# Kernel optimization log

Hardware: AMD Instinct MI355X
Metric: run time of the kernel (lower is better)

## Reference

```python
import jax, jax.numpy as jnp
import numpy as np

EPS = 1e-8
LN_EPS = 1e-5

def _ln(x, g, b):
    m = x.mean(-1, keepdims=True)
    v = ((x - m) ** 2).mean(-1, keepdims=True)
    return (x - m) * jax.lax.rsqrt(v + LN_EPS) * g + b

def _rbf(d, n_rbf):
    # standard protein RBF embedding: gaussians on [0, 20] Angstrom
    mu = jnp.linspace(0.0, 20.0, n_rbf)
    sigma = 20.0 / n_rbf
    return jnp.exp(-(((d[..., None] - mu) / sigma) ** 2))

def setup_inputs() -> dict:
    N, K, CS, CZ, G, RBF = 1024, 16, 256, 128, 16, 64
    key = jax.random.key(0)
    ks = jax.random.split(key, 24)
    s = 0.02
    inp = {
        'node_features': jax.random.normal(ks[0], (N, CS), jnp.float32),
        'trans': jax.random.normal(ks[1], (N, 3), jnp.float32) * 10.0,
        'src_edge_features': jax.random.normal(ks[2], (N, K, CZ), jnp.float32),
        'dst_edge_features': jax.random.normal(ks[3], (N, K, CZ), jnp.float32),
        # params
        'ln_src_g': jnp.ones((CZ,)), 'ln_src_b': jnp.zeros((CZ,)),
        'ln_dst_g': jnp.ones((CZ,)), 'ln_dst_b': jnp.zeros((CZ,)),
        'W_nl': jax.random.normal(ks[4], (G, CS)) * s, 'b_nl': jnp.zeros((G,)),
        'W_nr': jax.random.normal(ks[5], (G, CS)) * s, 'b_nr': jnp.zeros((G,)),
        'W_ep': jax.random.normal(ks[6], (CZ, CZ)) * s, 'b_ep': jnp.zeros((CZ,)),
        'W_eg': jax.random.normal(ks[7], (CZ, CZ)) * s, 'b_eg': jnp.zeros((CZ,)),
        'W_dg': jax.random.normal(ks[8], (CZ, G, G)) * s, 'b_dg': jnp.zeros((CZ,)),
        'W_dp': jax.random.normal(ks[9], (CZ, RBF)) * s, 'b_dp': jnp.zeros((CZ,)),
        'ln_out_g': jnp.ones((CZ,)), 'ln_out_b': jnp.zeros((CZ,)),
        'W_lo': jax.random.normal(ks[10], (CZ, CZ)) * s, 'b_lo': jnp.zeros((CZ,)),
        'W_og': jax.random.normal(ks[11], (CZ, CZ)) * s, 'b_og': jnp.zeros((CZ,)),
        # int / mask args (KNN form)
        'src_edge_index': jax.random.randint(ks[12], (2, N, K), 0, N, jnp.int32),
        'dst_edge_index': jax.random.randint(ks[13], (2, N, K), 0, N, jnp.int32),
        'src_mask': jnp.ones((N, K), bool),
        'dst_mask': jnp.ones((N, K), bool),
    }
    return inp

def reference(node_features, trans, src_edge_features, dst_edge_features,
              ln_src_g, ln_src_b, ln_dst_g, ln_dst_b,
              W_nl, b_nl, W_nr, b_nr, W_ep, b_ep, W_eg, b_eg,
              W_dg, b_dg, W_dp, b_dp, ln_out_g, ln_out_b,
              W_lo, b_lo, W_og, b_og,
              src_edge_index, dst_edge_index, src_mask, dst_mask):
    N, K, CZ = src_edge_features.shape
    src_ln = _ln(src_edge_features, ln_src_g, ln_src_b)   # [N,K,CZ]
    dst_ln = _ln(dst_edge_features, ln_dst_g, ln_dst_b)
    node_left = node_features @ W_nl.T + b_nl              # [N,G]
    node_right = node_features @ W_nr.T + b_nr
    e1 = node_left[src_edge_index[0]]                      # [N,K,G]
    e2 = node_right[dst_edge_index[0]]                     # [N,K,G]
    # triangle gate: fuse outer product [N,K,K,G,G] with dist_gate Linear
    t = jnp.einsum('nia,zab->nizb', e1, W_dg)
    gate3 = jnp.einsum('nizb,njb->nijz', t, e2) + b_dg     # [N,K,K,CZ]
    t1 = trans[src_edge_index[0]]                          # [N,K,3]
    t2 = trans[dst_edge_index[0]]
    d = jnp.linalg.norm(t1[:, :, None, :] - t2[:, None, :, :] + EPS, axis=-1)  # [N,K,K]
    distf = _rbf(d, W_dp.shape[1]) @ W_dp.T + b_dp         # [N,K,K,CZ]
    mask3 = (src_mask[:, :, None] & dst_mask[:, None, :])[..., None]
    edge3 = jax.nn.sigmoid(gate3) * distf * mask3          # [N,K,K,CZ]
    edge2 = jax.nn.sigmoid(src_ln @ W_eg.T + b_eg) * (src_ln @ W_ep.T + b_ep)  # [N,K,CZ]
    # batched per-channel combine: sum over dst slot j
    upd = jnp.einsum('nijz,njz->niz', edge3, edge2)        # [N,K,CZ]
    upd = _ln(upd, ln_out_g, ln_out_b) @ W_lo.T + b_lo
    upd = upd * jax.nn.sigmoid(dst_ln @ W_og.T + b_og)
    upd = upd * dst_mask[..., None]                        # knn -> sparse (masked flatten)
    return upd.reshape(N * K, CZ)
```

## Files before the change

### kernel.cpp

```cpp
#include <hip/hip_runtime.h>
#include <hip/hip_bf16.h>
#include <stdint.h>

#define N_    1024
#define K_    16
#define CZ_   128
#define G_    16
#define RBF_  64
#define CS_   256

typedef const float* fp;
typedef _Float16 f16x8 __attribute__((ext_vector_type(8)));
typedef _Float16 h2    __attribute__((ext_vector_type(2)));
typedef float f32x4    __attribute__((ext_vector_type(4)));

#define MFMA16(A,B,C) __builtin_amdgcn_mfma_f32_16x16x32_f16(A,B,C,0,0,0)

#define OFF_EGH 0
#define OFF_EPH 16384
#define OFF_OGH 32768
#define OFF_LOH 49152
#define OFF_DPH 65536
#define OFF_DGA 73728

__device__ __forceinline__ float sigm(float x){
  return __builtin_amdgcn_rcpf(1.0f + __expf(-x));
}
__device__ __forceinline__ unsigned short f2h(float v){
  union{_Float16 h; unsigned short u;} c; c.h = (_Float16)v; return c.u;
}
__device__ __forceinline__ float h2f(unsigned short u){
  union{unsigned short u; _Float16 h;} c; c.u = u; return (float)c.h;
}
__device__ __forceinline__ unsigned int pk2(float a, float b){
  union{h2 h; unsigned int u;} c; c.h[0] = (_Float16)a; c.h[1] = (_Float16)b; return c.u;
}
__device__ __forceinline__ f16x8 ldh8(const unsigned short* p){
  union{uint4 u; f16x8 h;} c; c.u = *(const uint4*)p; return c.h;
}
__device__ __forceinline__ f16x8 ldh8u(const unsigned short* p){
  union{uint2 u[2]; f16x8 h;} c;
  c.u[0] = *(const uint2*)p;
  c.u[1] = *(const uint2*)(p+4);
  return c.h;
}
__device__ __forceinline__ f16x8 cvt8(float4 a, float4 b){
  f16x8 r;
  r[0]=(_Float16)a.x; r[1]=(_Float16)a.y; r[2]=(_Float16)a.z; r[3]=(_Float16)a.w;
  r[4]=(_Float16)b.x; r[5]=(_Float16)b.y; r[6]=(_Float16)b.z; r[7]=(_Float16)b.w;
  return r;
}

__global__ __launch_bounds__(256) void repack(
    fp W_eg, fp W_ep, fp W_og, fp W_lo, fp W_dp, fp W_dg,
    unsigned short* __restrict__ ws)
{
  int t = blockIdx.x*256 + threadIdx.x;
  int stride = gridDim.x*256;
  for (int i = t; i < 16384; i += stride) {
    ws[OFF_EGH+i] = f2h(W_eg[i]);
    ws[OFF_EPH+i] = f2h(W_ep[i]);
    ws[OFF_OGH+i] = f2h(W_og[i]);
    ws[OFF_LOH+i] = f2h(W_lo[i]);
  }
  for (int i = t; i < 8192; i += stride)
    ws[OFF_DPH+i] = f2h(W_dp[i]);
  for (int i = t; i < 32768; i += stride) {
    int z = i >> 8, rem = i & 255;
    int l = rem >> 3, c = rem & 7;
    int a = ((l >> 4) << 3) | c;
    int b = l & 15;
    ws[OFF_DGA+i] = f2h(W_dg[z*256 + a*16 + b]);
  }
}

__global__ __launch_bounds__(512, 4) void tri_fused6(
    fp nf, fp trans, fp srcef, fp dstef,
    fp ln_src_g, fp ln_src_b, fp ln_dst_g, fp ln_dst_b,
    fp W_nl, fp b_nl, fp W_nr, fp b_nr,
    fp b_eg, fp b_ep, fp b_og,
    fp b_dg, fp b_dp, fp ln_out_g, fp ln_out_b, fp b_lo,
    const int* __restrict__ sidx, const int* __restrict__ didx,
    const unsigned short* __restrict__ ws,
    float* __restrict__ out)
{
  __shared__ __align__(16) unsigned char smem[72192];
  float*          updf   = (float*)smem;
  unsigned short* edge2h = (unsigned short*)(smem + 8448);
  unsigned short* sogh   = (unsigned short*)(smem + 13056);
  unsigned short* e1h    = (unsigned short*)(smem + 17152);
  unsigned short* e2h    = (unsigned short*)(smem + 17664);
  float (*t1f)[4]        = (float(*)[4])(smem + 18304);
  float (*t2f)[4]        = (float(*)[4])(smem + 18560);
  unsigned short* poolH  = (unsigned short*)(smem + 18816);
  unsigned short* srcH   = poolH;
  unsigned short* dstH   = poolH + 2176;
  unsigned short* t_lds  = poolH;
  unsigned short* rbfH   = poolH + 16448;
  unsigned short* updH   = poolH;

  const int n   = blockIdx.x;
  const int tid = threadIdx.x;
  const int wv  = tid >> 6;
  const int lnn = tid & 63;
  const int lm  = lnn & 15;
  const int lq  = lnn >> 4;
  const int zz0 = wv*16 + lm;

  const int pf_which = wv & 1;
  const int pf_h     = wv >> 1;
  int pf_idx = (pf_which ? didx : sidx)[n*K_ + lm];
  const float* pf_arow = nf + pf_idx*CS_ + pf_h*64 + lq*8;
  const float* pf_wrow = (pf_which ? W_nr : W_nl) + lm*CS_ + pf_h*64 + lq*8;
  float4 pa0 = *(const float4*)(pf_arow);
  float4 pa1 = *(const float4*)(pf_arow + 4);
  float4 pa2 = *(const float4*)(pf_arow + 32);
  float4 pa3 = *(const float4*)(pf_arow + 36);
  float4 pw0 = *(const float4*)(pf_wrow);
  float4 pw1 = *(const float4*)(pf_wrow + 4);
  float4 pw2 = *(const float4*)(pf_wrow + 32);
  float4 pw3 = *(const float4*)(pf_wrow + 36);
  f16x8 wegv0 = ldh8(ws + OFF_EGH + zz0*128 + lq*8);
  f16x8 weph0 = ldh8(ws + OFF_EPH + zz0*128 + lq*8);
  f16x8 wogv0 = ldh8(ws + OFF_OGH + zz0*128 + lq*8);

  if (tid < 32) {
    int k = tid & 15;
    int id2 = (tid < 16) ? sidx[n*K_ + k] : didx[n*K_ + k];
    float* tf = (tid < 16) ? &t1f[k][0] : &t2f[k][0];
    tf[0] = trans[id2*3+0]; tf[1] = trans[id2*3+1]; tf[2] = trans[id2*3+2];
  }
  {
    int row = tid >> 4;
    int c0  = (tid & 15) * 8;
    int r16 = row & 15;
    bool isSrc = row < 16;
    const float* base = (isSrc ? srcef : dstef) + (n*K_ + r16)*CZ_ + c0;
    float4 xa = *(const float4*)base;
    float4 xb = *(const float4*)(base+4);
    float x[8] = {xa.x,xa.y,xa.z,xa.w,xb.x,xb.y,xb.z,xb.w};
    float s = x[0]+x[1]+x[2]+x[3]+x[4]+x[5]+x[6]+x[7];
    s += __shfl_xor(s,1); s += __shfl_xor(s,2);
    s += __shfl_xor(s,4); s += __shfl_xor(s,8);
    float m = s * 0.0078125f;
    float q = 0.f;
    #pragma unroll
    for (int i = 0; i < 8; ++i) { float d = x[i]-m; q += d*d; }
    q += __shfl_xor(q,1); q += __shfl_xor(q,2);
    q += __shfl_xor(q,4); q += __shfl_xor(q,8);
    float rv = rsqrtf(q * 0.0078125f + 1e-5f);
    fp gp = isSrc ? ln_src_g : ln_dst_g;
    fp bp = isSrc ? ln_src_b : ln_dst_b;
    float y[8];
    #pragma unroll
    for (int i = 0; i < 8; ++i) y[i] = (x[i]-m)*rv*gp[c0+i] + bp[c0+i];
    uint4 uh;
    uh.x = pk2(y[0],y[1]); uh.y = pk2(y[2],y[3]); uh.z = pk2(y[4],y[5]); uh.w = pk2(y[6],y[7]);
    *(uint4*)&((isSrc ? srcH : dstH)[r16*136 + c0]) = uh;
  }
  __syncthreads();

  {
    f32x4 acc = {0.f,0.f,0.f,0.f};
    acc = MFMA16(cvt8(pa0,pa1), cvt8(pw0,pw1), acc);
    acc = MFMA16(cvt8(pa2,pa3), cvt8(pw2,pw3), acc);
    float* pst = (float*)updf;
    #pragma unroll
    for (int r = 0; r < 4; ++r)
      pst[wv*256 + r*64 + lnn] = acc[r];
  }

  {
    const int z = zz0;
    f32x4 aeg = {0.f,0.f,0.f,0.f}, aep = {0.f,0.f,0.f,0.f}, aog = {0.f,0.f,0.f,0.f};
    {
      f16x8 sh = ldh8(srcH + lm*136 + lq*8);
      f16x8 dh = ldh8(dstH + lm*136 + lq*8);
      aeg = MFMA16(sh, wegv0, aeg);
      aep = MFMA16(sh, weph0, aep);
      aog = MFMA16(dh, wogv0, aog);
    }
    #pragma unroll
    for (int kb = 32; kb < 128; kb += 32) {
      f16x8 sh = ldh8(srcH + lm*136 + kb + lq*8);
      f16x8 dh = ldh8(dstH + lm*136 + kb + lq*8);
      f16x8 wegv = ldh8(ws + OFF_EGH + z*128 + kb + lq*8);
      f16x8 weph = ldh8(ws + OFF_EPH + z*128 + kb + lq*8);
      f16x8 wogv = ldh8(ws + OFF_OGH + z*128 + kb + lq*8);
      aeg = MFMA16(sh, wegv, aeg);
      aep = MFMA16(sh, weph, aep);
      aog = MFMA16(dh, wogv, aog);
    }
    float beg = b_eg[z], bep = b_ep[z], bog = b_og[z];
    #pragma unroll
    for (int r = 0; r < 4; ++r) {
      int j = lq*4 + r;
      edge2h[z*18 + j] = f2h(sigm(aeg[r]+beg) * (aep[r]+bep));
      sogh[j*128 + z]  = f2h(sigm(aog[r]+bog));
    }
  }
  __syncthreads();

  if (wv < 2) {
    const float* pst = (const float*)updf;
    float bias = (wv ? b_nr : b_nl)[lm];
    #pragma unroll
    for (int r = 0; r < 4; ++r) {
      float v = pst[(wv  )*256 + r*64 + lnn]
              + pst[(wv+2)*256 + r*64 + lnn]
              + pst[(wv+4)*256 + r*64 + lnn]
              + pst[(wv+6)*256 + r*64 + lnn];
      v += bias;
      if (wv) e2h[(lq*4+r)*20 + lm] = f2h(v);
      else    e1h[(lq*4+r)*16 + lm] = f2h(v);
    }
  }
  __syncthreads();

  {
    const int z = zz0;
    f16x8 Bdp0 = ldh8(ws + OFF_DPH + z*64 + lq*8);
    f16x8 Bdp1 = ldh8(ws + OFF_DPH + z*64 + 32 + lq*8);
    const float bdg = b_dg[z], bdp = b_dp[z];
    float e2v4[4];
    #pragma unroll
    for (int r = 0; r < 4; ++r) e2v4[r] = h2f(edge2h[z*18 + lq*4 + r]);

    f16x8 zf = {(_Float16)0,(_Float16)0,(_Float16)0,(_Float16)0,
                (_Float16)0,(_Float16)0,(_Float16)0,(_Float16)0};
    f16x8 e1B = zf;
    f16x8 e2A = zf;
    if (lq < 2) {
      e1B = ldh8 (e1h + lm*16 + lq*8);
      e2A = ldh8u(e2h + lm*20 + lq*8);
    }
    const float inv_sigma = 3.2f;
    const float mustep = 20.0f/63.0f;

    for (int h = 0; h < 2; ++h) {
      __syncthreads();
      for (int zz = 0; zz < 16; ++zz) {
        int za = wv*16 + zz;
        f16x8 Ad = zf;
        if (lnn < 32) Ad = ldh8(ws + OFF_DGA + za*256 + lnn*8);
        f32x4 d4 = MFMA16(Ad, e1B, ((f32x4){0.f,0.f,0.f,0.f}));
        if ((lm >> 3) == h) {
          int ii = lm & 7;
          uint2 u;
          u.x = pk2(d4[0], d4[1]);
          u.y = pk2(d4[2], d4[3]);
          *(uint2*)&t_lds[ii*2056 + za*16 + lq*4] = u;
        }
      }
      {
        const int kh = wv & 1;
        #pragma unroll
        for (int p = 0; p < 2; ++p) {
          int slot = (wv >> 1) + p*4;
          int i = h*8 + slot;
          float dx = t1f[i][0]-t2f[lm][0]+1e-8f;
          float dy = t1f[i][1]-t2f[lm][1]+1e-8f;
          float dz = t1f[i][2]-t2f[lm][2]+1e-8f;
          float d = sqrtf(dx*dx+dy*dy+dz*dz);
          union { f16x8 hh; uint2 u2[2]; } cv;
          #pragma unroll
          for (int c = 0; c < 8; ++c) {
            int k = kh*32 + lq*8 + c;
            float tt = (d - (float)k*mustep) * inv_sigma;
            cv.hh[c] = (_Float16)__expf(-tt*tt);
          }
          unsigned short* dp = &rbfH[(slot*64+lnn)*20 + kh*8];
          *(uint2*)dp     = cv.u2[0];
          *(uint2*)(dp+4) = cv.u2[1];
        }
      }
      __syncthreads();

      for (int ii = 0; ii < 8; ++ii) {
        int i = h*8 + ii;
        f16x8 tB = zf;
        if (lq < 2) tB = ldh8(t_lds + ii*2056 + z*16 + lq*8);
        f32x4 accg = MFMA16(e2A, tB, ((f32x4){0.f,0.f,0.f,0.f}));
        const unsigned short* rp = &rbfH[(ii*64+lnn)*20];
        f16x8 r0 = ldh8u(rp);
        f16x8 r1 = ldh8u(rp + 8);
        f32x4 accp = {0.f,0.f,0.f,0.f};
        accp = MFMA16(r0, Bdp0, accp);
        accp = MFMA16(r1, Bdp1, accp);
        float s = 0.f;
        #pragma unroll
        for (int r = 0; r < 4; ++r)
          s += sigm(accg[r]+bdg) * (accp[r]+bdp) * e2v4[r];
        s += __shfl_xor(s,16); s += __shfl_xor(s,32);
        if (lq == 0) updf[i*132 + z] = s;
      }
    }
  }
  __syncthreads();

  {
    int row = tid >> 5;
    int c0  = (tid & 31) * 4;
    float4 x = *(const float4*)&updf[row*132 + c0];
    float s = x.x+x.y+x.z+x.w;
    s += __shfl_xor(s,1,32); s += __shfl_xor(s,2,32); s += __shfl_xor(s,4,32);
    s += __shfl_xor(s,8,32); s += __shfl_xor(s,16,32);
    float m = s * 0.0078125f;
    float q = (x.x-m)*(x.x-m)+(x.y-m)*(x.y-m)+(x.z-m)*(x.z-m)+(x.w-m)*(x.w-m);
    q += __shfl_xor(q,1,32); q += __shfl_xor(q,2,32); q += __shfl_xor(q,4,32);
    q += __shfl_xor(q,8,32); q += __shfl_xor(q,16,32);
    float rv = rsqrtf(q*0.0078125f + 1e-5f);
    float y0 = (x.x-m)*rv*ln_out_g[c0+0] + ln_out_b[c0+0];
    float y1 = (x.y-m)*rv*ln_out_g[c0+1] + ln_out_b[c0+1];
    float y2 = (x.z-m)*rv*ln_out_g[c0+2] + ln_out_b[c0+2];
    float y3 = (x.w-m)*rv*ln_out_g[c0+3] + ln_out_b[c0+3];
    uint2 uh;
    uh.x = pk2(y0,y1); uh.y = pk2(y2,y3);
    *(uint2*)&updH[row*136 + c0] = uh;
  }
  __syncthreads();

  {
    const int z = zz0;
    f32x4 acc = {0.f,0.f,0.f,0.f};
    #pragma unroll
    for (int kb = 0; kb < 128; kb += 32) {
      f16x8 ah = ldh8(updH + lm*136 + kb + lq*8);
      f16x8 bh = ldh8(ws + OFF_LOH + z*128 + kb + lq*8);
      acc = MFMA16(ah, bh, acc);
    }
    float blo = b_lo[z];
    #pragma unroll
    for (int r = 0; r < 4; ++r) {
      int islot = lq*4 + r;
      out[(n*K_ + islot)*CZ_ + z] = (acc[r] + blo) * h2f(sogh[islot*128 + z]);
    }
  }
}

extern "C" void kernel_launch(void* const* d_in, const int* in_sizes, int n_in,
                              void* d_out, int out_size, void* d_ws, size_t ws_size,
                              hipStream_t stream)
{
  fp nodef    = (fp)d_in[0];
  fp trans    = (fp)d_in[1];
  fp srcef    = (fp)d_in[2];
  fp dstef    = (fp)d_in[3];
  fp ln_src_g = (fp)d_in[4];  fp ln_src_b = (fp)d_in[5];
  fp ln_dst_g = (fp)d_in[6];  fp ln_dst_b = (fp)d_in[7];
  fp W_nl = (fp)d_in[8];   fp b_nl = (fp)d_in[9];
  fp W_nr = (fp)d_in[10];  fp b_nr = (fp)d_in[11];
  fp W_ep = (fp)d_in[12];  fp b_ep = (fp)d_in[13];
  fp W_eg = (fp)d_in[14];  fp b_eg = (fp)d_in[15];
  fp W_dg = (fp)d_in[16];  fp b_dg = (fp)d_in[17];
  fp W_dp = (fp)d_in[18];  fp b_dp = (fp)d_in[19];
  fp ln_out_g = (fp)d_in[20]; fp ln_out_b = (fp)d_in[21];
  fp W_lo = (fp)d_in[22];  fp b_lo = (fp)d_in[23];
  fp W_og = (fp)d_in[24];  fp b_og = (fp)d_in[25];
  const int* sidx = (const int*)d_in[26];
  const int* didx = (const int*)d_in[27];

  unsigned short* ws16 = (unsigned short*)d_ws;
  float* outp = (float*)d_out;

  hipLaunchKernelGGL(repack, dim3(64), dim3(256), 0, stream,
                     W_eg, W_ep, W_og, W_lo, W_dp, W_dg, ws16);
  hipLaunchKernelGGL(tri_fused6, dim3(N_), dim3(512), 0, stream,
                     nodef, trans, srcef, dstef,
                     ln_src_g, ln_src_b, ln_dst_g, ln_dst_b,
                     W_nl, b_nl, W_nr, b_nr,
                     b_eg, b_ep, b_og,
                     b_dg, b_dp, ln_out_g, ln_out_b, b_lo,
                     sidx, didx, ws16, outp);
}
```

Measured before the change: 182.4 us.

## Double-buffer triangle-gate and RBF staging across quarters to overlap producer and consumer

Splits the 16 source slots into four quarters with ping-pong LDS buffers for the gate intermediate and the RBF tiles. The next quarter's gate MFMAs and RBF exp computation are interleaved with the current quarter's consume MFMAs, so each quarter needs one barrier instead of two per half. The aim is to hide LDS write, barrier and transcendental latency behind MFMA work. In exchange, the stage-A gate MFMAs are now recomputed per quarter rather than per half, roughly doubling that work, and the LDS pool is packed to the full allocation.

```diff
diff --git a/kernel.cpp b/kernel.cpp
--- a/kernel.cpp
+++ b/kernel.cpp
@@ -95,8 +95,10 @@
   unsigned short* poolH  = (unsigned short*)(smem + 18816);
   unsigned short* srcH   = poolH;
   unsigned short* dstH   = poolH + 2176;
-  unsigned short* t_lds  = poolH;
-  unsigned short* rbfH   = poolH + 16448;
+  unsigned short* t0p    = poolH;
+  unsigned short* rbf0p  = poolH + 8224;
+  unsigned short* t1p    = poolH + 13344;
+  unsigned short* rbf1p  = poolH + 21568;
   unsigned short* updH   = poolH;
 
   const int n   = blockIdx.x;
@@ -237,66 +239,82 @@
     const float inv_sigma = 3.2f;
     const float mustep = 20.0f/63.0f;
 
-    for (int h = 0; h < 2; ++h) {
-      __syncthreads();
-      for (int zz = 0; zz < 16; ++zz) {
+    auto stageA4 = [&](int qq, unsigned short* tp, int k4) {
+      #pragma unroll
+      for (int zz = k4*4; zz < k4*4+4; ++zz) {
         int za = wv*16 + zz;
         f16x8 Ad = zf;
         if (lnn < 32) Ad = ldh8(ws + OFF_DGA + za*256 + lnn*8);
         f32x4 d4 = MFMA16(Ad, e1B, ((f32x4){0.f,0.f,0.f,0.f}));
-        if ((lm >> 3) == h) {
-          int ii = lm & 7;
+        if ((lm >> 2) == qq) {
+          int ii = lm & 3;
           uint2 u;
           u.x = pk2(d4[0], d4[1]);
           u.y = pk2(d4[2], d4[3]);
-          *(uint2*)&t_lds[ii*2056 + za*16 + lq*4] = u;
+          *(uint2*)&tp[ii*2056 + za*16 + lq*4] = u;
         }
       }
-      {
-        const int kh = wv & 1;
+    };
+    auto produceR = [&](int qq, unsigned short* rp) {
+      const int kh = wv & 1;
+      int slot = wv >> 1;
+      int i = qq*4 + slot;
+      float dx = t1f[i][0]-t2f[lm][0]+1e-8f;
+      float dy = t1f[i][1]-t2f[lm][1]+1e-8f;
+      float dz = t1f[i][2]-t2f[lm][2]+1e-8f;
+      float d = sqrtf(dx*dx+dy*dy+dz*dz);
+      union { f16x8 hh; uint2 u2[2]; } cv;
+      #pragma unroll
+      for (int c = 0; c < 8; ++c) {
+        int k = kh*32 + lq*8 + c;
+        float tt = (d - (float)k*mustep) * inv_sigma;
+        cv.hh[c] = (_Float16)__expf(-tt*tt);
+      }
+      unsigned short* dp = &rp[(slot*64+lnn)*20 + kh*8];
+      *(uint2*)dp     = cv.u2[0];
+      *(uint2*)(dp+4) = cv.u2[1];
+    };
+    auto consumeB = [&](int q, int ii, unsigned short* tc, unsigned short* rc) {
+      int i = q*4 + ii;
+      f16x8 tB = zf;
+      if (lq < 2) tB = ldh8(tc + ii*2056 + z*16 + lq*8);
+      f32x4 accg = MFMA16(e2A, tB, ((f32x4){0.f,0.f,0.f,0.f}));
+      const unsigned short* rr = &rc[(ii*64+lnn)*20];
+      f16x8 r0 = ldh8u(rr);
+      f16x8 r1 = ldh8u(rr + 8);
+      f32x4 accp = {0.f,0.f,0.f,0.f};
+      accp = MFMA16(r0, Bdp0, accp);
+      accp = MFMA16(r1, Bdp1, accp);
+      float s = 0.f;
+      #pragma unroll
+      for (int r = 0; r < 4; ++r)
+        s += sigm(accg[r]+bdg) * (accp[r]+bdp) * e2v4[r];
+      s += __shfl_xor(s,16); s += __shfl_xor(s,32);
+      if (lq == 0) updf[i*132 + z] = s;
+    };
+
+    stageA4(0, t0p, 0); stageA4(0, t0p, 1); stageA4(0, t0p, 2); stageA4(0, t0p, 3);
+    produceR(0, rbf0p);
+    __syncthreads();
+    for (int q = 0; q < 4; ++q) {
+      unsigned short* tc = (q & 1) ? t1p  : t0p;
+      unsigned short* rc = (q & 1) ? rbf1p: rbf0p;
+      unsigned short* tp = (q & 1) ? t0p  : t1p;
+      unsigned short* rp = (q & 1) ? rbf0p: rbf1p;
+      if (q < 3) {
         #pragma unroll
-        for (int p = 0; p < 2; ++p) {
-          int slot = (wv >> 1) + p*4;
-          int i = h*8 + slot;
-          float dx = t1f[i][0]-t2f[lm][0]+1e-8f;
-          float dy = t1f[i][1]-t2f[lm][1]+1e-8f;
-          float dz = t1f[i][2]-t2f[lm][2]+1e-8f;
-          float d = sqrtf(dx*dx+dy*dy+dz*dz);
-          union { f16x8 hh; uint2 u2[2]; } cv;
-          #pragma unroll
-          for (int c = 0; c < 8; ++c) {
-            int k = kh*32 + lq*8 + c;
-            float tt = (d - (float)k*mustep) * inv_sigma;
-            cv.hh[c] = (_Float16)__expf(-tt*tt);
-          }
-          unsigned short* dp = &rbfH[(slot*64+lnn)*20 + kh*8];
-          *(uint2*)dp     = cv.u2[0];
-          *(uint2*)(dp+4) = cv.u2[1];
+        for (int k = 0; k < 4; ++k) {
+          stageA4(q+1, tp, k);
+          consumeB(q, k, tc, rc);
         }
+        produceR(q+1, rp);
+      } else {
+        #pragma unroll
+        for (int k = 0; k < 4; ++k) consumeB(q, k, tc, rc);
       }
       __syncthreads();
-
-      for (int ii = 0; ii < 8; ++ii) {
-        int i = h*8 + ii;
-        f16x8 tB = zf;
-        if (lq < 2) tB = ldh8(t_lds + ii*2056 + z*16 + lq*8);
-        f32x4 accg = MFMA16(e2A, tB, ((f32x4){0.f,0.f,0.f,0.f}));
-        const unsigned short* rp = &rbfH[(ii*64+lnn)*20];
-        f16x8 r0 = ldh8u(rp);
-        f16x8 r1 = ldh8u(rp + 8);
-        f32x4 accp = {0.f,0.f,0.f,0.f};
-        accp = MFMA16(r0, Bdp0, accp);
-        accp = MFMA16(r1, Bdp1, accp);
-        float s = 0.f;
-        #pragma unroll
-        for (int r = 0; r < 4; ++r)
-          s += sigm(accg[r]+bdg) * (accp[r]+bdp) * e2v4[r];
-        s += __shfl_xor(s,16); s += __shfl_xor(s,32);
-        if (lq == 0) updf[i*132 + z] = s;
-      }
-    }
-  }
-  __syncthreads();
+    }
+  }
 
   {
     int row = tid >> 5;
```

Result: slower. 189.9 us (+4.1%).
